# Performance work log

Measured on AMD Instinct MI355X. Metric: run time of the kernel, lower is better.

Reference implementation:

```python
import jax, jax.numpy as jnp
import numpy as np

_LEVELS = jnp.array([-4, -2, -1, 0, 1, 2, 4], dtype=jnp.int32)  # shift-quant 7-value grid 'A'

B, S = 1, 512
IN_F, OUT_F = 4096, 16384
BLOCK = 64
NUM_BLOCKS = (IN_F + BLOCK - 1) // BLOCK  # 64


def setup_inputs() -> dict:
    key = jax.random.key(0)
    k1, k2, k3, k4 = jax.random.split(key, 4)
    x = jax.random.normal(k1, (B, S, IN_F), dtype=jnp.float32)
    idx = jax.random.randint(k2, (OUT_F, IN_F), 0, 7)
    q_weight = _LEVELS[idx]  # int32 values in {-4,-2,-1,0,1,2,4}
    scales = (jax.random.uniform(k3, (OUT_F, NUM_BLOCKS), dtype=jnp.float32) * 0.05 + 0.001).astype(jnp.float16)
    bias = (jax.random.normal(k4, (OUT_F,), dtype=jnp.float32) * 0.02).astype(jnp.float16)
    return {"x": x, "q_weight": q_weight, "scales": scales, "bias": bias, "block_size": BLOCK}


def reference(x, q_weight, scales, bias, block_size):
    # shift_matmul: dequantize blockwise-scaled power-of-two int8 weights, then GEMM.
    out_f, in_f = q_weight.shape
    # broadcast per-block fp16 scales along the in_features axis (handles padding block)
    w_scale = jnp.repeat(scales.astype(jnp.float32), block_size, axis=1)[:, :in_f]  # [out, in]
    w = q_weight.astype(jnp.float32) * w_scale  # [out, in]
    out = jnp.einsum("bsi,oi->bso", x, w)
    out = out + bias.astype(out.dtype)
    return out.astype(x.dtype)
```

## Files before the change

### kernel.cpp

```cpp
#include <hip/hip_runtime.h>
#include <hip/hip_bf16.h>
#include <stdint.h>


#define MM 512
#define NN 16384
#define KK 4096
#define BN 64
#define BK 128
#define NKB (KK / BK)

typedef __bf16 bf16x8 __attribute__((ext_vector_type(8)));
typedef float floatx4 __attribute__((ext_vector_type(4)));

__device__ __forceinline__ void barrier_nodrain() {
    asm volatile("s_waitcnt lgkmcnt(0)\n\ts_barrier" ::: "memory");
}

__device__ __forceinline__ unsigned int pk_bf16_rtn(float lo, float hi) {
    __hip_bfloat162 h = __float22bfloat162_rn(float2{lo, hi});
    return *reinterpret_cast<unsigned int*>(&h);
}

__global__ __launch_bounds__(256) void pack_x(const float* __restrict__ x,
                                              unsigned short* __restrict__ xp) {
    const int t    = blockIdx.x * 256 + threadIdx.x;
    const int lane = t & 63;
    const int mt   = (t >> 6) & 31;
    const int ks   = (t >> 11) & 3;
    const int kb   = t >> 13;
    const int m    = mt * 16 + (lane & 15);
    const int k    = kb * 128 + ks * 32 + (lane >> 4) * 8;
    const float* px = x + (size_t)m * KK + k;
    const float4 a = *(const float4*)px;
    const float4 b = *(const float4*)(px + 4);
    uint4 o;
    o.x = pk_bf16_rtn(a.x, a.y);
    o.y = pk_bf16_rtn(a.z, a.w);
    o.z = pk_bf16_rtn(b.x, b.y);
    o.w = pk_bf16_rtn(b.z, b.w);
    *(uint4*)(xp + (size_t)t * 8) = o;
}

template <bool PRE>
__global__ __launch_bounds__(1024, 4) void qlin_gemm(
    const float* __restrict__ xf,
    const unsigned short* __restrict__ xp,
    const int* __restrict__ qw,
    const float* __restrict__ scales,
    const float* __restrict__ bias,
    float* __restrict__ out)
{
    __shared__ unsigned short sB[2][BN * BK];

    const int t    = threadIdx.x;
    const int lane = t & 63;
    const int w    = t >> 6;
    const int ln   = lane & 15;
    const int quad = lane >> 4;
    const int n0   = blockIdx.x * BN;

    const int r    = t >> 4;
    const int oct  = t & 15;
    const int ksp  = oct >> 2;
    const int jp   = r >> 4;
    const int ldst = (((oct & 3) << 4) | (r & 15)) ^ (ksp << 1);
    const int woff = ((ksp * 4 + jp) * 64 + ldst) * 8;
    const int* qp  = qw + (size_t)(n0 + r) * KK + oct * 8;
    const float* sp = scales + (size_t)(n0 + r) * 64 + (oct >> 3);

    floatx4 acc[2][4];
#pragma unroll
    for (int i = 0; i < 2; ++i)
#pragma unroll
        for (int j = 0; j < 4; ++j)
            acc[i][j] = (floatx4)0.0f;

    int4 qv0 = *(const int4*)(qp);
    int4 qv1 = *(const int4*)(qp + 4);
    float s  = sp[0];

    bf16x8 a[2][4][2];
    if constexpr (PRE) {
#pragma unroll
        for (int ks = 0; ks < 4; ++ks) {
            const unsigned short* ap = xp + (size_t)((ks * 32 + w * 2) * 64 + lane) * 8;
            a[0][ks][0] = *(const bf16x8*)(ap);
            a[0][ks][1] = *(const bf16x8*)(ap + 512);
        }
    }

#pragma unroll 2
    for (int kb = 0; kb < NKB; ++kb) {
        const int cur = kb & 1;
        unsigned short* sb = sB[cur];

        uint4 u;
        u.x = pk_bf16_rtn((float)qv0.x * s, (float)qv0.y * s);
        u.y = pk_bf16_rtn((float)qv0.z * s, (float)qv0.w * s);
        u.z = pk_bf16_rtn((float)qv1.x * s, (float)qv1.y * s);
        u.w = pk_bf16_rtn((float)qv1.z * s, (float)qv1.w * s);
        *(uint4*)(sb + woff) = u;

        barrier_nodrain();

        if (kb + 1 < NKB) {
            qv0 = *(const int4*)(qp + (size_t)(kb + 1) * BK);
            qv1 = *(const int4*)(qp + (size_t)(kb + 1) * BK + 4);
            s   = sp[(size_t)(kb + 1) * 2];
            if constexpr (PRE) {
                const unsigned short* xpb = xp + (size_t)(kb + 1) * (4 * 32 * 64 * 8);
#pragma unroll
                for (int ks = 0; ks < 4; ++ks) {
                    const unsigned short* ap = xpb + (size_t)((ks * 32 + w * 2) * 64 + lane) * 8;
                    a[cur ^ 1][ks][0] = *(const bf16x8*)(ap);
                    a[cur ^ 1][ks][1] = *(const bf16x8*)(ap + 512);
                }
            }
        }

#pragma unroll
        for (int ks = 0; ks < 4; ++ks) {
            bf16x8 a0, a1;
            if constexpr (PRE) {
                a0 = a[cur][ks][0];
                a1 = a[cur][ks][1];
            } else {
                const int k = kb * BK + ks * 32 + quad * 8;
#pragma unroll
                for (int i = 0; i < 2; ++i) {
                    const float* px = xf + (size_t)(w * 32 + i * 16 + ln) * KK + k;
                    const float4 f0 = *(const float4*)px;
                    const float4 f1 = *(const float4*)(px + 4);
                    uint4 ua;
                    ua.x = pk_bf16_rtn(f0.x, f0.y);
                    ua.y = pk_bf16_rtn(f0.z, f0.w);
                    ua.z = pk_bf16_rtn(f1.x, f1.y);
                    ua.w = pk_bf16_rtn(f1.z, f1.w);
                    if (i == 0) a0 = *(bf16x8*)&ua; else a1 = *(bf16x8*)&ua;
                }
            }
            bf16x8 bfr[4];
#pragma unroll
            for (int j = 0; j < 4; ++j)
                bfr[j] = *(const bf16x8*)(sb + ((ks * 4 + j) * 64 + (lane ^ (ks << 1))) * 8);
#pragma unroll
            for (int j = 0; j < 4; ++j) {
                acc[0][j] = __builtin_amdgcn_mfma_f32_16x16x32_bf16(a0, bfr[j], acc[0][j], 0, 0, 0);
                acc[1][j] = __builtin_amdgcn_mfma_f32_16x16x32_bf16(a1, bfr[j], acc[1][j], 0, 0, 0);
            }
        }
    }

#pragma unroll
    for (int j = 0; j < 4; ++j) {
        const int n = n0 + j * 16 + ln;
        const float bv = bias[n];
#pragma unroll
        for (int i = 0; i < 2; ++i) {
            const int mbase = w * 32 + i * 16 + quad * 4;
#pragma unroll
            for (int rr = 0; rr < 4; ++rr)
                out[(size_t)(mbase + rr) * NN + n] = acc[i][j][rr] + bv;
        }
    }
}

extern "C" void kernel_launch(void* const* d_in, const int* in_sizes, int n_in,
                              void* d_out, int out_size, void* d_ws, size_t ws_size,
                              hipStream_t stream) {
    const float* x    = (const float*)d_in[0];
    const int* qw     = (const int*)d_in[1];
    const float* scl  = (const float*)d_in[2];
    const float* bias = (const float*)d_in[3];
    float* out        = (float*)d_out;

    dim3 grid(NN / BN);
    dim3 block(1024);

    if (ws_size >= (size_t)MM * KK * sizeof(unsigned short)) {
        unsigned short* xp = (unsigned short*)d_ws;
        pack_x<<<dim3(MM * KK / (256 * 8)), dim3(256), 0, stream>>>(x, xp);
        qlin_gemm<true><<<grid, block, 0, stream>>>(x, xp, qw, scl, bias, out);
    } else {
        qlin_gemm<false><<<grid, block, 0, stream>>>(x, nullptr, qw, scl, bias, out);
    }
}
```

Measured before the change: 417.0 us.

## Software-pipeline weight dequant one stage ahead with double-buffered LDS and deeper prefetch

The K loop is restructured so each iteration dequantizes and stores the next tile's weights into the other LDS buffer before computing on the current one. Global weight loads are prefetched two iterations ahead, and the barrier moves to the end of the iteration. The intent is to overlap dequantization and LDS writes with MFMA work and hide global load latency behind more compute. The LDS B-fragment loads are also interleaved with the MFMAs in pairs to lower register pressure. In exchange it keeps more values live in registers, and manual unrolling through a macro raises code size.

```diff
diff --git a/kernel.cpp b/kernel.cpp
--- a/kernel.cpp
+++ b/kernel.cpp
@@ -20,6 +20,15 @@
 __device__ __forceinline__ unsigned int pk_bf16_rtn(float lo, float hi) {
     __hip_bfloat162 h = __float22bfloat162_rn(float2{lo, hi});
     return *reinterpret_cast<unsigned int*>(&h);
+}
+
+__device__ __forceinline__ uint4 deq8(const int4 q0, const int4 q1, const float s) {
+    uint4 u;
+    u.x = pk_bf16_rtn((float)q0.x * s, (float)q0.y * s);
+    u.y = pk_bf16_rtn((float)q0.z * s, (float)q0.w * s);
+    u.z = pk_bf16_rtn((float)q1.x * s, (float)q1.y * s);
+    u.w = pk_bf16_rtn((float)q1.z * s, (float)q1.w * s);
+    return u;
 }
 
 __global__ __launch_bounds__(256) void pack_x(const float* __restrict__ x,
@@ -42,6 +51,72 @@
     *(uint4*)(xp + (size_t)t * 8) = o;
 }
 
+#define GEMM_ITER(KB, CUR)                                                          \
+    {                                                                               \
+        const unsigned short* sb = sB[(CUR)];                                       \
+        unsigned short* sbw      = sB[(CUR) ^ 1];                                   \
+        if ((KB) + 1 < NKB) {                                                       \
+                  \
+               \
+            uint4 u = deq8(qv0, qv1, s);                                            \
+            *(uint4*)(sbw + woff) = u;                                              \
+                                \
+            if constexpr (PRE) {                                                    \
+                const unsigned short* xpb =                                         \
+                    xp + (size_t)((KB) + 1) * (4 * 32 * 64 * 8);                    \
+                _Pragma("unroll")                                                   \
+                for (int ks = 0; ks < 4; ++ks) {                                    \
+                    const unsigned short* ap =                                      \
+                        xpb + (size_t)((ks * 32 + w * 2) * 64 + lane) * 8;          \
+                    a[(CUR) ^ 1][ks][0] = *(const bf16x8*)(ap);                     \
+                    a[(CUR) ^ 1][ks][1] = *(const bf16x8*)(ap + 512);               \
+                }                                                                   \
+            }                                                                       \
+        }                                                                           \
+        if ((KB) + 2 < NKB) {                                                       \
+                    \
+            qv0 = *(const int4*)(qp + (size_t)((KB) + 2) * BK);                     \
+            qv1 = *(const int4*)(qp + (size_t)((KB) + 2) * BK + 4);                 \
+            s   = sp[(size_t)((KB) + 2) * 2];                                       \
+        }                                                                           \
+                 \
+        _Pragma("unroll")                                                           \
+        for (int ks = 0; ks < 4; ++ks) {                                            \
+            bf16x8 a0, a1;                                                          \
+            if constexpr (PRE) {                                                    \
+                a0 = a[(CUR)][ks][0];                                               \
+                a1 = a[(CUR)][ks][1];                                               \
+            } else {                                                                \
+                const int k = (KB) * BK + ks * 32 + quad * 8;                       \
+                _Pragma("unroll")                                                   \
+                for (int i = 0; i < 2; ++i) {                                       \
+                    const float* px = xf + (size_t)(w * 32 + i * 16 + ln) * KK + k; \
+                    const float4 f0 = *(const float4*)px;                           \
+                    const float4 f1 = *(const float4*)(px + 4);                     \
+                    uint4 ua;                                                       \
+                    ua.x = pk_bf16_rtn(f0.x, f0.y);                                 \
+                    ua.y = pk_bf16_rtn(f0.z, f0.w);                                 \
+                    ua.z = pk_bf16_rtn(f1.x, f1.y);                                 \
+                    ua.w = pk_bf16_rtn(f1.z, f1.w);                                 \
+                    if (i == 0) a0 = *(bf16x8*)&ua; else a1 = *(bf16x8*)&ua;        \
+                }                                                                   \
+            }                                                                       \
+            const int sl = lane ^ (ks << 1);                                        \
+            _Pragma("unroll")                                                       \
+            for (int jj = 0; jj < 4; jj += 2) {                                     \
+                bf16x8 b0 = *(const bf16x8*)(sb + ((ks * 4 + jj) * 64 + sl) * 8);   \
+                bf16x8 b1 = *(const bf16x8*)(sb + ((ks * 4 + jj + 1) * 64 + sl) * 8);\
+                acc[0][jj]     = __builtin_amdgcn_mfma_f32_16x16x32_bf16(a0, b0, acc[0][jj], 0, 0, 0);     \
+                acc[1][jj]     = __builtin_amdgcn_mfma_f32_16x16x32_bf16(a1, b0, acc[1][jj], 0, 0, 0);     \
+                acc[0][jj + 1] = __builtin_amdgcn_mfma_f32_16x16x32_bf16(a0, b1, acc[0][jj + 1], 0, 0, 0); \
+                acc[1][jj + 1] = __builtin_amdgcn_mfma_f32_16x16x32_bf16(a1, b1, acc[1][jj + 1], 0, 0, 0); \
+            }                                                                       \
+        }                                                                           \
+            \
+                  \
+        if ((KB) + 1 < NKB) barrier_nodrain();                                      \
+    }
+
 template <bool PRE>
 __global__ __launch_bounds__(1024, 4) void qlin_gemm(
     const float* __restrict__ xf,
@@ -89,67 +164,18 @@
             a[0][ks][1] = *(const bf16x8*)(ap + 512);
         }
     }
-
-#pragma unroll 2
-    for (int kb = 0; kb < NKB; ++kb) {
-        const int cur = kb & 1;
-        unsigned short* sb = sB[cur];
-
-        uint4 u;
-        u.x = pk_bf16_rtn((float)qv0.x * s, (float)qv0.y * s);
-        u.y = pk_bf16_rtn((float)qv0.z * s, (float)qv0.w * s);
-        u.z = pk_bf16_rtn((float)qv1.x * s, (float)qv1.y * s);
-        u.w = pk_bf16_rtn((float)qv1.z * s, (float)qv1.w * s);
-        *(uint4*)(sb + woff) = u;
-
-        barrier_nodrain();
-
-        if (kb + 1 < NKB) {
-            qv0 = *(const int4*)(qp + (size_t)(kb + 1) * BK);
-            qv1 = *(const int4*)(qp + (size_t)(kb + 1) * BK + 4);
-            s   = sp[(size_t)(kb + 1) * 2];
-            if constexpr (PRE) {
-                const unsigned short* xpb = xp + (size_t)(kb + 1) * (4 * 32 * 64 * 8);
-#pragma unroll
-                for (int ks = 0; ks < 4; ++ks) {
-                    const unsigned short* ap = xpb + (size_t)((ks * 32 + w * 2) * 64 + lane) * 8;
-                    a[cur ^ 1][ks][0] = *(const bf16x8*)(ap);
-                    a[cur ^ 1][ks][1] = *(const bf16x8*)(ap + 512);
-                }
-            }
-        }
-
-#pragma unroll
-        for (int ks = 0; ks < 4; ++ks) {
-            bf16x8 a0, a1;
-            if constexpr (PRE) {
-                a0 = a[cur][ks][0];
-                a1 = a[cur][ks][1];
-            } else {
-                const int k = kb * BK + ks * 32 + quad * 8;
-#pragma unroll
-                for (int i = 0; i < 2; ++i) {
-                    const float* px = xf + (size_t)(w * 32 + i * 16 + ln) * KK + k;
-                    const float4 f0 = *(const float4*)px;
-                    const float4 f1 = *(const float4*)(px + 4);
-                    uint4 ua;
-                    ua.x = pk_bf16_rtn(f0.x, f0.y);
-                    ua.y = pk_bf16_rtn(f0.z, f0.w);
-                    ua.z = pk_bf16_rtn(f1.x, f1.y);
-                    ua.w = pk_bf16_rtn(f1.z, f1.w);
-                    if (i == 0) a0 = *(bf16x8*)&ua; else a1 = *(bf16x8*)&ua;
-                }
-            }
-            bf16x8 bfr[4];
-#pragma unroll
-            for (int j = 0; j < 4; ++j)
-                bfr[j] = *(const bf16x8*)(sb + ((ks * 4 + j) * 64 + (lane ^ (ks << 1))) * 8);
-#pragma unroll
-            for (int j = 0; j < 4; ++j) {
-                acc[0][j] = __builtin_amdgcn_mfma_f32_16x16x32_bf16(a0, bfr[j], acc[0][j], 0, 0, 0);
-                acc[1][j] = __builtin_amdgcn_mfma_f32_16x16x32_bf16(a1, bfr[j], acc[1][j], 0, 0, 0);
-            }
-        }
+    {
+        uint4 u = deq8(qv0, qv1, s);
+        *(uint4*)(sB[0] + woff) = u;
+    }
+    qv0 = *(const int4*)(qp + BK);
+    qv1 = *(const int4*)(qp + BK + 4);
+    s   = sp[2];
+    barrier_nodrain();
+
+    for (int kb = 0; kb < NKB; kb += 2) {
+        GEMM_ITER(kb, 0)
+        GEMM_ITER(kb + 1, 1)
     }
 
 #pragma unroll
```

Result: no change. 422.3 us (+1.3%).

## Split each N-tile across two 512-thread blocks over M halves

Applied to the files above, without the earlier changes.

Block size drops from 1024 to 512 threads and the grid doubles. Each block now covers one half of M for a 64-column N tile, so each thread dequantizes two weight rows instead of one. The A-fragment register double-buffering is dropped: A is loaded at the start of each iteration, and the weight prefetch now happens before the barrier. This should give more, smaller blocks for better scheduling and occupancy. The cost is that every weight tile is dequantized twice, once per M-half, which doubles weight global reads and dequant work.

```diff
diff --git a/kernel.cpp b/kernel.cpp
--- a/kernel.cpp
+++ b/kernel.cpp
@@ -20,6 +20,15 @@
 __device__ __forceinline__ unsigned int pk_bf16_rtn(float lo, float hi) {
     __hip_bfloat162 h = __float22bfloat162_rn(float2{lo, hi});
     return *reinterpret_cast<unsigned int*>(&h);
+}
+
+__device__ __forceinline__ uint4 deq8(const int4 q0, const int4 q1, const float s) {
+    uint4 u;
+    u.x = pk_bf16_rtn((float)q0.x * s, (float)q0.y * s);
+    u.y = pk_bf16_rtn((float)q0.z * s, (float)q0.w * s);
+    u.z = pk_bf16_rtn((float)q1.x * s, (float)q1.y * s);
+    u.w = pk_bf16_rtn((float)q1.z * s, (float)q1.w * s);
+    return u;
 }
 
 __global__ __launch_bounds__(256) void pack_x(const float* __restrict__ x,
@@ -43,7 +52,7 @@
 }
 
 template <bool PRE>
-__global__ __launch_bounds__(1024, 4) void qlin_gemm(
+__global__ __launch_bounds__(512, 4) void qlin_gemm(
     const float* __restrict__ xf,
     const unsigned short* __restrict__ xp,
     const int* __restrict__ qw,
@@ -58,7 +67,8 @@
     const int w    = t >> 6;
     const int ln   = lane & 15;
     const int quad = lane >> 4;
-    const int n0   = blockIdx.x * BN;
+    const int h    = blockIdx.x & 1;
+    const int n0   = (blockIdx.x >> 1) * BN;
 
     const int r    = t >> 4;
     const int oct  = t & 15;
@@ -66,8 +76,10 @@
     const int jp   = r >> 4;
     const int ldst = (((oct & 3) << 4) | (r & 15)) ^ (ksp << 1);
     const int woff = ((ksp * 4 + jp) * 64 + ldst) * 8;
-    const int* qp  = qw + (size_t)(n0 + r) * KK + oct * 8;
-    const float* sp = scales + (size_t)(n0 + r) * 64 + (oct >> 3);
+    const int* qp0   = qw + (size_t)(n0 + r) * KK + oct * 8;
+    const int* qp1   = qp0 + (size_t)32 * KK;
+    const float* sp0 = scales + (size_t)(n0 + r) * 64 + (oct >> 3);
+    const float* sp1 = sp0 + 32 * 64;
 
     floatx4 acc[2][4];
 #pragma unroll
@@ -76,60 +88,59 @@
         for (int j = 0; j < 4; ++j)
             acc[i][j] = (floatx4)0.0f;
 
-    int4 qv0 = *(const int4*)(qp);
-    int4 qv1 = *(const int4*)(qp + 4);
-    float s  = sp[0];
-
-    bf16x8 a[2][4][2];
-    if constexpr (PRE) {
-#pragma unroll
-        for (int ks = 0; ks < 4; ++ks) {
-            const unsigned short* ap = xp + (size_t)((ks * 32 + w * 2) * 64 + lane) * 8;
-            a[0][ks][0] = *(const bf16x8*)(ap);
-            a[0][ks][1] = *(const bf16x8*)(ap + 512);
-        }
-    }
-
-#pragma unroll 2
+    int4 qa0 = *(const int4*)(qp0);
+    int4 qa1 = *(const int4*)(qp0 + 4);
+    int4 qb0 = *(const int4*)(qp1);
+    int4 qb1 = *(const int4*)(qp1 + 4);
+    float sa = sp0[0];
+    float sc = sp1[0];
+
+    bf16x8 a[4][2];
+
     for (int kb = 0; kb < NKB; ++kb) {
-        const int cur = kb & 1;
-        unsigned short* sb = sB[cur];
-
-        uint4 u;
-        u.x = pk_bf16_rtn((float)qv0.x * s, (float)qv0.y * s);
-        u.y = pk_bf16_rtn((float)qv0.z * s, (float)qv0.w * s);
-        u.z = pk_bf16_rtn((float)qv1.x * s, (float)qv1.y * s);
-        u.w = pk_bf16_rtn((float)qv1.z * s, (float)qv1.w * s);
-        *(uint4*)(sb + woff) = u;
+        unsigned short* sbuf = sB[kb & 1];
+
+        if constexpr (PRE) {
+            const unsigned short* xpb = xp + (size_t)kb * (4 * 32 * 64 * 8);
+#pragma unroll
+            for (int ks = 0; ks < 4; ++ks) {
+                const unsigned short* ap =
+                    xpb + (size_t)((ks * 32 + h * 16 + w * 2) * 64 + lane) * 8;
+                a[ks][0] = *(const bf16x8*)(ap);
+                a[ks][1] = *(const bf16x8*)(ap + 512);
+            }
+        }
+
+        {
+            uint4 u0 = deq8(qa0, qa1, sa);
+            uint4 u1 = deq8(qb0, qb1, sc);
+            *(uint4*)(sbuf + woff)        = u0;
+            *(uint4*)(sbuf + woff + 1024) = u1;
+        }
+
+        if (kb + 1 < NKB) {
+            qa0 = *(const int4*)(qp0 + (size_t)(kb + 1) * BK);
+            qa1 = *(const int4*)(qp0 + (size_t)(kb + 1) * BK + 4);
+            qb0 = *(const int4*)(qp1 + (size_t)(kb + 1) * BK);
+            qb1 = *(const int4*)(qp1 + (size_t)(kb + 1) * BK + 4);
+            sa = sp0[(size_t)(kb + 1) * 2];
+            sc = sp1[(size_t)(kb + 1) * 2];
+        }
 
         barrier_nodrain();
-
-        if (kb + 1 < NKB) {
-            qv0 = *(const int4*)(qp + (size_t)(kb + 1) * BK);
-            qv1 = *(const int4*)(qp + (size_t)(kb + 1) * BK + 4);
-            s   = sp[(size_t)(kb + 1) * 2];
-            if constexpr (PRE) {
-                const unsigned short* xpb = xp + (size_t)(kb + 1) * (4 * 32 * 64 * 8);
-#pragma unroll
-                for (int ks = 0; ks < 4; ++ks) {
-                    const unsigned short* ap = xpb + (size_t)((ks * 32 + w * 2) * 64 + lane) * 8;
-                    a[cur ^ 1][ks][0] = *(const bf16x8*)(ap);
-                    a[cur ^ 1][ks][1] = *(const bf16x8*)(ap + 512);
-                }
-            }
-        }
 
 #pragma unroll
         for (int ks = 0; ks < 4; ++ks) {
             bf16x8 a0, a1;
             if constexpr (PRE) {
-                a0 = a[cur][ks][0];
-                a1 = a[cur][ks][1];
+                a0 = a[ks][0];
+                a1 = a[ks][1];
             } else {
                 const int k = kb * BK + ks * 32 + quad * 8;
 #pragma unroll
                 for (int i = 0; i < 2; ++i) {
-                    const float* px = xf + (size_t)(w * 32 + i * 16 + ln) * KK + k;
+                    const float* px =
+                        xf + (size_t)(h * 256 + w * 32 + i * 16 + ln) * KK + k;
                     const float4 f0 = *(const float4*)px;
                     const float4 f1 = *(const float4*)(px + 4);
                     uint4 ua;
@@ -140,14 +151,15 @@
                     if (i == 0) a0 = *(bf16x8*)&ua; else a1 = *(bf16x8*)&ua;
                 }
             }
-            bf16x8 bfr[4];
-#pragma unroll
-            for (int j = 0; j < 4; ++j)
-                bfr[j] = *(const bf16x8*)(sb + ((ks * 4 + j) * 64 + (lane ^ (ks << 1))) * 8);
-#pragma unroll
-            for (int j = 0; j < 4; ++j) {
-                acc[0][j] = __builtin_amdgcn_mfma_f32_16x16x32_bf16(a0, bfr[j], acc[0][j], 0, 0, 0);
-                acc[1][j] = __builtin_amdgcn_mfma_f32_16x16x32_bf16(a1, bfr[j], acc[1][j], 0, 0, 0);
+            const int sl = lane ^ (ks << 1);
+#pragma unroll
+            for (int jj = 0; jj < 4; jj += 2) {
+                bf16x8 b0 = *(const bf16x8*)(sbuf + ((ks * 4 + jj) * 64 + sl) * 8);
+                bf16x8 b1 = *(const bf16x8*)(sbuf + ((ks * 4 + jj + 1) * 64 + sl) * 8);
+                acc[0][jj]     = __builtin_amdgcn_mfma_f32_16x16x32_bf16(a0, b0, acc[0][jj], 0, 0, 0);
+                acc[1][jj]     = __builtin_amdgcn_mfma_f32_16x16x32_bf16(a1, b0, acc[1][jj], 0, 0, 0);
+                acc[0][jj + 1] = __builtin_amdgcn_mfma_f32_16x16x32_bf16(a0, b1, acc[0][jj + 1], 0, 0, 0);
+                acc[1][jj + 1] = __builtin_amdgcn_mfma_f32_16x16x32_bf16(a1, b1, acc[1][jj + 1], 0, 0, 0);
             }
         }
     }
@@ -158,7 +170,7 @@
         const float bv = bias[n];
 #pragma unroll
         for (int i = 0; i < 2; ++i) {
-            const int mbase = w * 32 + i * 16 + quad * 4;
+            const int mbase = h * 256 + w * 32 + i * 16 + quad * 4;
 #pragma unroll
             for (int rr = 0; rr < 4; ++rr)
                 out[(size_t)(mbase + rr) * NN + n] = acc[i][j][rr] + bv;
@@ -175,8 +187,8 @@
     const float* bias = (const float*)d_in[3];
     float* out        = (float*)d_out;
 
-    dim3 grid(NN / BN);
-    dim3 block(1024);
+    dim3 grid(NN / BN * 2);
+    dim3 block(512);
 
     if (ws_size >= (size_t)MM * KK * sizeof(unsigned short)) {
         unsigned short* xp = (unsigned short*)d_ws;
```

New measurement: 442.2 us. 6.1% more time.
